# Performance work log

Measured on AMD Instinct MI355X. Metric: run time of the kernel, lower is better.

## Reference

```python
import jax, jax.numpy as jnp
import numpy as np

NFILTS = 6  # module-level global in the original repo


def setup_inputs() -> dict:
    key = jax.random.key(0)
    k = jax.random.split(key, 6)
    N, T, D, E = 128, 256, 10, NFILTS
    merged = jax.random.normal(k[0], (N, T, 14), dtype=jnp.float32)
    y_pred_i = jax.random.normal(k[1], (N, T, E), dtype=jnp.float32)
    y_pred_ij = jax.random.normal(k[2], (N, N, T, E), dtype=jnp.float32)
    # input1 holds flux errors in channels [1+nfilts : -2]; keep them bounded away from 0
    input1 = jax.random.uniform(k[3], (N, T, 1 + E + E + 2), dtype=jnp.float32) + 0.5
    samples = jax.random.normal(k[4], (N, D), dtype=jnp.float32)
    labels = jax.random.randint(k[5], (N,), 0, 10, dtype=jnp.int64)
    return {"merged": merged, "y_pred_i": y_pred_i, "y_pred_ij": y_pred_ij,
            "input1": input1, "samples": samples, "labels": labels}


def reference(merged, y_pred_i, y_pred_ij, input1, samples, labels):
    # err_true: [N, T, E]
    err_true = input1[:, :, 1 + NFILTS:-2]
    # pairwise latent distance: S_ij[i,j] = mean_d (samples[j] - samples[i])^2 -> [N, N]
    d = samples[None, :, :] - samples[:, None, :]
    S_ij = jnp.mean(d * d, axis=-1)
    # second term: mean over (T, E) of (y_pred_ij[i,j] - y_pred_i[j])^2 / err_true[j]^2 / 10
    diffsq = jnp.square(y_pred_ij - y_pred_i[None, :, :, :])          # [N, N, T, E]
    second = jnp.mean(diffsq / jnp.square(err_true)[None], axis=(2, 3)) / 10.0  # [N, N]
    avg_term = 0.5 * (second + second.T)
    L_sim = jnp.mean(jnp.abs(S_ij - avg_term))
    return L_sim
```

## Files before the change

kernel.cpp:

```cpp
#include <hip/hip_runtime.h>
#include <hip/hip_bf16.h>

#define NN 128
#define TT 256
#define EE 6
#define DD 10
#define TE (TT*EE)
#define C1 15

__global__ void prep_w(const float* __restrict__ input1, float* __restrict__ w) {
    int idx = blockIdx.x * 256 + threadIdx.x;
    if (idx < NN * TE) {
        int f = idx % TE;
        int j = idx / TE;
        int t = f / EE, e = f % EE;
        float v = input1[(j * TT + t) * C1 + 1 + EE + e];
        w[idx] = 1.0f / (v * v);
    }
}

__launch_bounds__(128)
__global__ void pair_reduce(const float* __restrict__ yij,
                            const float* __restrict__ yi,
                            const float* __restrict__ w,
                            float* __restrict__ raw) {
    const int j = blockIdx.x;
    const int i = blockIdx.y;
    const int tid = threadIdx.x;

    const float4* a  = (const float4*)(yij + ((size_t)i * NN + j) * TE);
    const float4* m  = (const float4*)(yi  + (size_t)j * TE);
    const float4* wv = (const float4*)(w   + (size_t)j * TE);

    float s = 0.0f;
#pragma unroll
    for (int k = 0; k < 3; ++k) {
        int f = tid + k * 128;
        float4 x  = a[f];
        float4 mm = m[f];
        float4 ww = wv[f];
        float d0 = x.x - mm.x; s += d0 * d0 * ww.x;
        float d1 = x.y - mm.y; s += d1 * d1 * ww.y;
        float d2 = x.z - mm.z; s += d2 * d2 * ww.z;
        float d3 = x.w - mm.w; s += d3 * d3 * ww.w;
    }
#pragma unroll
    for (int off = 32; off > 0; off >>= 1) s += __shfl_down(s, off);

    __shared__ float ls[2];
    if ((tid & 63) == 0) ls[tid >> 6] = s;
    __syncthreads();
    if (tid == 0) raw[i * NN + j] = ls[0] + ls[1];
}

__launch_bounds__(256)
__global__ void finalize(const float* __restrict__ raw,
                         const float* __restrict__ samples,
                         float* __restrict__ out) {
    __shared__ float smp[NN * DD];
    for (int k = threadIdx.x; k < NN * DD; k += 256) smp[k] = samples[k];
    __syncthreads();

    const int p = blockIdx.x * 256 + threadIdx.x;
    const int i = p / NN, j = p % NN;

    float S = 0.0f;
#pragma unroll
    for (int d = 0; d < DD; ++d) {
        float dd = smp[j * DD + d] - smp[i * DD + d];
        S += dd * dd;
    }
    S *= (1.0f / DD);

    const float sec = (raw[i * NN + j] + raw[j * NN + i]) * (0.5f / (TE * 10.0f));
    float v = fabsf(S - sec);

#pragma unroll
    for (int off = 32; off > 0; off >>= 1) v += __shfl_down(v, off);

    __shared__ float ls[4];
    const int tid = threadIdx.x;
    if ((tid & 63) == 0) ls[tid >> 6] = v;
    __syncthreads();
    if (tid == 0)
        atomicAdd(out, (ls[0] + ls[1] + ls[2] + ls[3]) * (1.0f / (NN * NN)));
}

extern "C" void kernel_launch(void* const* d_in, const int* in_sizes, int n_in,
                              void* d_out, int out_size, void* d_ws, size_t ws_size,
                              hipStream_t stream) {
    const float* y_pred_i  = (const float*)d_in[1];
    const float* y_pred_ij = (const float*)d_in[2];
    const float* input1    = (const float*)d_in[3];
    const float* samples   = (const float*)d_in[4];
    float* out = (float*)d_out;

    float* w   = (float*)d_ws;
    float* raw = w + (size_t)NN * TE;

    prep_w<<<(NN * TE + 255) / 256, 256, 0, stream>>>(input1, w);

    dim3 grid(NN, NN);
    pair_reduce<<<grid, 128, 0, stream>>>(y_pred_ij, y_pred_i, w, raw);

    hipMemsetAsync(out, 0, sizeof(float), stream);
    finalize<<<64, 256, 0, stream>>>(raw, samples, out);
}
```

Baseline: 162.4 us.

## Fuse pair reduction and finalize via last-block counter, reuse per-j weights across rows

Merges the pairwise reduction and final reduction kernels into one. The last-arriving block, found through an atomic counter, computes the final mean, which removes a kernel launch and the memset. Each block now handles 16 i-rows for one j, with each wavefront covering 4 rows. It keeps y_pred_i and the weights for that j in registers, cutting redundant loads and block count. The cost is a serial tail in which one block processes all 16K pairs, plus extra register pressure.

```diff
diff --git a/kernel.cpp b/kernel.cpp
--- a/kernel.cpp
+++ b/kernel.cpp
@@ -6,10 +6,14 @@
 #define EE 6
 #define DD 10
 #define TE (TT*EE)
+#define F4 (TE/4)
 #define C1 15
+#define NBLK (NN*8)
 
-__global__ void prep_w(const float* __restrict__ input1, float* __restrict__ w) {
+__global__ void prep_w(const float* __restrict__ input1, float* __restrict__ w,
+                       unsigned int* __restrict__ cnt) {
     int idx = blockIdx.x * 256 + threadIdx.x;
+    if (idx == 0) *cnt = 0u;
     if (idx < NN * TE) {
         int f = idx % TE;
         int j = idx / TE;
@@ -19,71 +23,83 @@
     }
 }
 
-__launch_bounds__(128)
-__global__ void pair_reduce(const float* __restrict__ yij,
-                            const float* __restrict__ yi,
-                            const float* __restrict__ w,
-                            float* __restrict__ raw) {
-    const int j = blockIdx.x;
-    const int i = blockIdx.y;
-    const int tid = threadIdx.x;
+__launch_bounds__(256)
+__global__ void pair_reduce_finalize(const float* __restrict__ yij,
+                                     const float* __restrict__ yi,
+                                     const float* __restrict__ w,
+                                     const float* __restrict__ samples,
+                                     float* __restrict__ raw,
+                                     unsigned int* __restrict__ cnt,
+                                     float* __restrict__ out) {
+    const int j    = blockIdx.x;
+    const int i0   = blockIdx.y * 16;
+    const int tid  = threadIdx.x;
+    const int wv   = tid >> 6;
+    const int lane = tid & 63;
 
-    const float4* a  = (const float4*)(yij + ((size_t)i * NN + j) * TE);
-    const float4* m  = (const float4*)(yi  + (size_t)j * TE);
-    const float4* wv = (const float4*)(w   + (size_t)j * TE);
+    const float4* m4 = (const float4*)(yi + (size_t)j * TE);
+    const float4* w4 = (const float4*)(w  + (size_t)j * TE);
+    float4 ym[6], wm[6];
+#pragma unroll
+    for (int m = 0; m < 6; ++m) {
+        ym[m] = m4[lane + 64 * m];
+        wm[m] = w4[lane + 64 * m];
+    }
 
-    float s = 0.0f;
 #pragma unroll
-    for (int k = 0; k < 3; ++k) {
-        int f = tid + k * 128;
-        float4 x  = a[f];
-        float4 mm = m[f];
-        float4 ww = wv[f];
-        float d0 = x.x - mm.x; s += d0 * d0 * ww.x;
-        float d1 = x.y - mm.y; s += d1 * d1 * ww.y;
-        float d2 = x.z - mm.z; s += d2 * d2 * ww.z;
-        float d3 = x.w - mm.w; s += d3 * d3 * ww.w;
+    for (int k = 0; k < 4; ++k) {
+        const int i = i0 + wv * 4 + k;
+        const float4* a = (const float4*)(yij + ((size_t)i * NN + j) * TE);
+        float s = 0.0f;
+#pragma unroll
+        for (int m = 0; m < 6; ++m) {
+            float4 x = a[lane + 64 * m];
+            float d0 = x.x - ym[m].x; s += d0 * d0 * wm[m].x;
+            float d1 = x.y - ym[m].y; s += d1 * d1 * wm[m].y;
+            float d2 = x.z - ym[m].z; s += d2 * d2 * wm[m].z;
+            float d3 = x.w - ym[m].w; s += d3 * d3 * wm[m].w;
+        }
+#pragma unroll
+        for (int off = 32; off > 0; off >>= 1) s += __shfl_down(s, off);
+        if (lane == 0) raw[(size_t)i * NN + j] = s;
+    }
+
+    __shared__ int isLast;
+    __syncthreads();
+    if (tid == 0) {
+        __threadfence();
+        unsigned int old = atomicAdd(cnt, 1u);
+        isLast = (old == NBLK - 1) ? 1 : 0;
+    }
+    __syncthreads();
+    if (!isLast) return;
+    __threadfence();
+
+    __shared__ float smp[NN * DD];
+    for (int q = tid; q < NN * DD; q += 256) smp[q] = samples[q];
+    __syncthreads();
+
+    float acc = 0.0f;
+    for (int it = 0; it < 64; ++it) {
+        const int p  = it * 256 + tid;
+        const int i  = p >> 7, jj = p & 127;
+        float S = 0.0f;
+#pragma unroll
+        for (int d = 0; d < DD; ++d) {
+            float dd = smp[jj * DD + d] - smp[i * DD + d];
+            S += dd * dd;
+        }
+        S *= (1.0f / DD);
+        float sec = (raw[p] + raw[jj * NN + i]) * (0.5f / (TE * 10.0f));
+        acc += fabsf(S - sec);
     }
 #pragma unroll
-    for (int off = 32; off > 0; off >>= 1) s += __shfl_down(s, off);
-
-    __shared__ float ls[2];
-    if ((tid & 63) == 0) ls[tid >> 6] = s;
-    __syncthreads();
-    if (tid == 0) raw[i * NN + j] = ls[0] + ls[1];
-}
-
-__launch_bounds__(256)
-__global__ void finalize(const float* __restrict__ raw,
-                         const float* __restrict__ samples,
-                         float* __restrict__ out) {
-    __shared__ float smp[NN * DD];
-    for (int k = threadIdx.x; k < NN * DD; k += 256) smp[k] = samples[k];
-    __syncthreads();
-
-    const int p = blockIdx.x * 256 + threadIdx.x;
-    const int i = p / NN, j = p % NN;
-
-    float S = 0.0f;
-#pragma unroll
-    for (int d = 0; d < DD; ++d) {
-        float dd = smp[j * DD + d] - smp[i * DD + d];
-        S += dd * dd;
-    }
-    S *= (1.0f / DD);
-
-    const float sec = (raw[i * NN + j] + raw[j * NN + i]) * (0.5f / (TE * 10.0f));
-    float v = fabsf(S - sec);
-
-#pragma unroll
-    for (int off = 32; off > 0; off >>= 1) v += __shfl_down(v, off);
-
+    for (int off = 32; off > 0; off >>= 1) acc += __shfl_down(acc, off);
     __shared__ float ls[4];
-    const int tid = threadIdx.x;
-    if ((tid & 63) == 0) ls[tid >> 6] = v;
+    if ((tid & 63) == 0) ls[tid >> 6] = acc;
     __syncthreads();
     if (tid == 0)
-        atomicAdd(out, (ls[0] + ls[1] + ls[2] + ls[3]) * (1.0f / (NN * NN)));
+        out[0] = (ls[0] + ls[1] + ls[2] + ls[3]) * (1.0f / (NN * NN));
 }
 
 extern "C" void kernel_launch(void* const* d_in, const int* in_sizes, int n_in,
@@ -97,12 +113,11 @@
 
     float* w   = (float*)d_ws;
     float* raw = w + (size_t)NN * TE;
+    unsigned int* cnt = (unsigned int*)(raw + (size_t)NN * NN);
 
-    prep_w<<<(NN * TE + 255) / 256, 256, 0, stream>>>(input1, w);
+    prep_w<<<(NN * TE + 255) / 256, 256, 0, stream>>>(input1, w, cnt);
 
-    dim3 grid(NN, NN);
-    pair_reduce<<<grid, 128, 0, stream>>>(y_pred_ij, y_pred_i, w, raw);
-
-    hipMemsetAsync(out, 0, sizeof(float), stream);
-    finalize<<<64, 256, 0, stream>>>(raw, samples, out);
+    dim3 grid(NN, 8);
+    pair_reduce_finalize<<<grid, 256, 0, stream>>>(y_pred_ij, y_pred_i, w,
+                                                   samples, raw, cnt, out);
 }
```

New measurement: 221.0 us. +36.1%, slower.
